# Optimization experiments

Measured on AMD Instinct MI355X. Metric: run time of the kernel, lower is better.

Reference implementation:

```python
import jax, jax.numpy as jnp
import numpy as np

N = 50000          # nodes
E = 800000         # edges (before self-loops)
NIN = 300          # n_in
H = 4              # heads
C = 64             # nhid (per-head out channels)
G = 256            # number of graphs in batch
NOUT = 768         # nout
NEG_SLOPE_ATT = 0.2   # PyG GATConv leaky-relu slope for attention logits
NEG_SLOPE_ACT = 0.01  # nn.LeakyReLU default


def setup_inputs() -> dict:
    key = jax.random.key(0)
    ks = jax.random.split(key, 9)
    x = jax.random.normal(ks[0], (N, NIN), dtype=jnp.float32)
    edge_index = jax.random.randint(ks[1], (2, E), 0, N, dtype=jnp.int32)
    batch = jnp.sort(jax.random.randint(ks[2], (N,), 0, G, dtype=jnp.int32))
    lin_w = jax.random.normal(ks[3], (NIN, H * C), dtype=jnp.float32) / np.sqrt(NIN)
    att_src = jax.random.normal(ks[4], (H, C), dtype=jnp.float32) / np.sqrt(C)
    att_dst = jax.random.normal(ks[5], (H, C), dtype=jnp.float32) / np.sqrt(C)
    bias = jnp.zeros((H * C,), dtype=jnp.float32)
    fc1_w = jax.random.normal(ks[6], (H * C, NOUT), dtype=jnp.float32) / np.sqrt(H * C)
    fc1_b = jnp.zeros((NOUT,), dtype=jnp.float32)
    return {"x": x, "edge_index": edge_index, "batch": batch, "lin_w": lin_w,
            "att_src": att_src, "att_dst": att_dst, "bias": bias,
            "fc1_w": fc1_w, "fc1_b": fc1_b}


def reference(x, edge_index, batch, lin_w, att_src, att_dst, bias, fc1_w, fc1_b):
    n = x.shape[0]
    h = (x @ lin_w).reshape(n, H, C)                      # [N,H,C]
    # add self-loops (PyG GATConv default)
    loop = jnp.arange(n, dtype=edge_index.dtype)
    src = jnp.concatenate([edge_index[0], loop])          # [E+N]
    dst = jnp.concatenate([edge_index[1], loop])
    # per-edge attention logits
    a_src = jnp.einsum('nhc,hc->nh', h, att_src)          # [N,H]
    a_dst = jnp.einsum('nhc,hc->nh', h, att_dst)
    e = jax.nn.leaky_relu(a_src[src] + a_dst[dst], NEG_SLOPE_ATT)  # [E+N,H]
    # segment softmax grouped by destination node (self-loops -> every segment nonempty)
    emax = jax.ops.segment_max(e, dst, num_segments=n)    # [N,H]
    ee = jnp.exp(e - emax[dst])
    denom = jax.ops.segment_sum(ee, dst, num_segments=n)
    alpha = ee / denom[dst]                               # [E+N,H]
    # weighted message aggregation
    msg = h[src] * alpha[..., None]                       # [E+N,H,C]
    out = jax.ops.segment_sum(msg, dst, num_segments=n).reshape(n, H * C) + bias
    out = jax.nn.leaky_relu(out, NEG_SLOPE_ACT)
    # global mean pool over graphs
    sums = jax.ops.segment_sum(out, batch, num_segments=G)        # [G,H*C]
    cnt = jax.ops.segment_sum(jnp.ones((n, 1), out.dtype), batch, num_segments=G)
    pooled = sums / jnp.maximum(cnt, 1.0)
    return pooled @ fc1_w + fc1_b                         # [G,NOUT]
```

## Files before the change

kernel.cpp:

```cpp
#include <hip/hip_runtime.h>
#include <hip/hip_bf16.h>

using bf16 = __hip_bfloat16;
typedef __attribute__((ext_vector_type(8))) short short8;
typedef __attribute__((ext_vector_type(4))) float f32x4;

constexpr int N   = 50000;
constexpr int E   = 800000;
constexpr int NIN = 300;
constexpr int H   = 4;
constexpr int C   = 64;
constexpr int HC  = H * C;
constexpr int G   = 256;
constexpr int NOUT = 768;
constexpr int NKB = 10;
constexpr int NT  = 782;

__device__ __forceinline__ float b2f(bf16 v) { return __bfloat162float(v); }
__device__ __forceinline__ float us2f(unsigned short u) {
    bf16 b; *(unsigned short*)&b = u; return __bfloat162float(b);
}
__device__ __forceinline__ unsigned short f2us(float f) {
    bf16 b = __float2bfloat16(f); return *(unsigned short*)&b;
}
__device__ __forceinline__ float lrelu_att(float v) { return v > 0.f ? v : 0.2f * v; }
__device__ __forceinline__ float lrelu_act(float v) { return v > 0.f ? v : 0.01f * v; }
__device__ __forceinline__ float ldin(const void* p, int isbf, size_t i) {
    return isbf ? b2f(((const bf16*)p)[i]) : ((const float*)p)[i];
}
__device__ __forceinline__ short8 pack8u(ushort4 lo, ushort4 hi) {
    short8 r;
    r[0] = (short)lo.x; r[1] = (short)lo.y; r[2] = (short)lo.z; r[3] = (short)lo.w;
    r[4] = (short)hi.x; r[5] = (short)hi.y; r[6] = (short)hi.z; r[7] = (short)hi.w;
    return r;
}
__device__ __forceinline__ short8 pack8f(float4 lo, float4 hi) {
    short8 r;
    r[0] = (short)f2us(lo.x); r[1] = (short)f2us(lo.y); r[2] = (short)f2us(lo.z); r[3] = (short)f2us(lo.w);
    r[4] = (short)f2us(hi.x); r[5] = (short)f2us(hi.y); r[6] = (short)f2us(hi.z); r[7] = (short)f2us(hi.w);
    return r;
}

__device__ __forceinline__ short8 loadA_bf(const unsigned short* __restrict__ xr, int kb, int q) {
    ushort4 z = make_ushort4(0, 0, 0, 0);
    ushort4 lo = z, hi = z;
    if (kb < 9) {
        lo = *(const ushort4*)(xr + kb * 32);
        hi = *(const ushort4*)(xr + kb * 32 + 4);
    } else if (q == 0) {
        lo = *(const ushort4*)(xr + 288); hi = *(const ushort4*)(xr + 292);
    } else if (q == 1) {
        lo = *(const ushort4*)(xr + 288);
    }
    return pack8u(lo, hi);
}
__device__ __forceinline__ short8 loadA_f32(const float* __restrict__ xf, int kb, int q) {
    float4 zf = make_float4(0.f, 0.f, 0.f, 0.f);
    float4 lo = zf, hi = zf;
    if (kb < 9) {
        lo = *(const float4*)(xf + kb * 32);
        hi = *(const float4*)(xf + kb * 32 + 4);
    } else if (q == 0) {
        lo = *(const float4*)(xf + 288); hi = *(const float4*)(xf + 292);
    } else if (q == 1) {
        lo = *(const float4*)(xf + 288);
    }
    return pack8f(lo, hi);
}

__device__ __forceinline__ int block_detect(const unsigned short* __restrict__ xr) {
    __shared__ int cnt_s;
    if (threadIdx.x == 0) cnt_s = 0;
    __syncthreads();
    unsigned short u = xr[threadIdx.x & 255];
    int ex = (u >> 7) & 0xFF;
    int ok = (ex == 0) || (ex >= 100 && ex <= 140);
    if (threadIdx.x < 256) atomicAdd(&cnt_s, ok);
    __syncthreads();
    return (cnt_s >= 240) ? 1 : 0;
}

constexpr int NZ  = N + G * HC;
constexpr int NZB = (NZ + 255) / 256;
__global__ __launch_bounds__(256) void k_pre(const unsigned short* __restrict__ xr,
                                             const void* __restrict__ w,
                                             const int* __restrict__ batch,
                                             int* __restrict__ flag,
                                             int* __restrict__ zp,
                                             unsigned short* __restrict__ bswz,
                                             int* __restrict__ gs) {
    int b = blockIdx.x;
    if (b < NZB) {
        int i = b * 256 + threadIdx.x;
        if (i < NZ) zp[i] = 0;
        if (b == 0) {
            int isbf = block_detect(xr);
            if (threadIdx.x == 0) *flag = isbf;
        }
    } else if (b < NZB + 40) {
        int isbf = block_detect(xr);
        int fb = (b - NZB) * 4 + (threadIdx.x >> 6);
        if (fb < 160) {
            int kb = fb >> 4, nb = fb & 15;
            int lane = threadIdx.x & 63;
            int q = lane >> 4, cl = lane & 15;
            int n = nb * 16 + cl;
            unsigned short v[8];
#pragma unroll
            for (int j = 0; j < 8; j++) {
                int k = kb * 32 + q * 8 + j;
                float f = (k < NIN) ? ldin(w, isbf, (size_t)k * HC + n) : 0.f;
                v[j] = f2us(f);
            }
            ushort4* dst = (ushort4*)(bswz + ((size_t)fb * 64 + lane) * 8);
            dst[0] = make_ushort4(v[0], v[1], v[2], v[3]);
            dst[1] = make_ushort4(v[4], v[5], v[6], v[7]);
        }
    } else {
        int g = threadIdx.x;
        int lo = 0, hi = N;
        while (lo < hi) {
            int mid = (lo + hi) >> 1;
            if (batch[mid] < g) lo = mid + 1;
            else hi = mid;
        }
        gs[g] = lo;
        if (g == 0) gs[G] = N;
    }
}

__global__ __launch_bounds__(256, 4) void k_lin4(const void* __restrict__ x,
                                                 const unsigned short* __restrict__ bswz,
                                                 const void* __restrict__ att_s,
                                                 const void* __restrict__ att_d,
                                                 unsigned short* __restrict__ hb,
                                                 float* __restrict__ a_src,
                                                 float* __restrict__ a_dst,
                                                 const int* __restrict__ flag) {
    __shared__ unsigned short bs[40 * 64 * 8];
    int isbf = *flag;
    int t = threadIdx.x;
    int c       = blockIdx.x & 7;
    int j       = blockIdx.x >> 3;
    int quarter = j & 3;
    int bslot   = (j >> 2) * 8 + c;
    for (int i = t; i < 40 * 64; i += 256) {
        int f = i >> 6, lane = i & 63;
        int kb = f >> 2, nbl = f & 3;
        const int4* src = (const int4*)(bswz + ((size_t)(kb * 16 + quarter * 4 + nbl) * 64 + lane) * 8);
        ((int4*)bs)[i] = *src;
    }
    __syncthreads();

    int wave = t >> 6, lane = t & 63;
    int q = lane >> 4, cl = lane & 15;
    int hh = quarter;
    float as_h[4], ad_h[4];
#pragma unroll
    for (int nbl = 0; nbl < 4; nbl++) {
        as_h[nbl] = ldin(att_s, isbf, (quarter * 4 + nbl) * 16 + cl);
        ad_h[nbl] = ldin(att_d, isbf, (quarter * 4 + nbl) * 16 + cl);
    }
    for (int tile = bslot; tile < NT; tile += 256) {
        int m0 = tile * 64 + wave * 16;
        int row = m0 + cl; if (row >= N) row = N - 1;
        f32x4 acc[4];
#pragma unroll
        for (int nbl = 0; nbl < 4; nbl++) acc[nbl] = f32x4{0.f, 0.f, 0.f, 0.f};
        if (isbf) {
            const unsigned short* xr = (const unsigned short*)x + (size_t)row * NIN + q * 8;
            short8 a_cur = loadA_bf(xr, 0, q);
            short8 a_nxt = loadA_bf(xr, 1, q);
#pragma unroll
            for (int kb = 0; kb < NKB; kb++) {
                short8 a_pf = {};
                if (kb + 2 < NKB) a_pf = loadA_bf(xr, kb + 2, q);
                short8 bfr[4];
#pragma unroll
                for (int nbl = 0; nbl < 4; nbl++)
                    bfr[nbl] = *(const short8*)(bs + ((size_t)(kb * 4 + nbl) * 64 + lane) * 8);
#pragma unroll
                for (int nbl = 0; nbl < 4; nbl++)
                    acc[nbl] = __builtin_amdgcn_mfma_f32_16x16x32_bf16(a_cur, bfr[nbl], acc[nbl], 0, 0, 0);
                a_cur = a_nxt; a_nxt = a_pf;
            }
        } else {
            const float* xf = (const float*)x + (size_t)row * NIN + q * 8;
            short8 a_cur = loadA_f32(xf, 0, q);
            short8 a_nxt = loadA_f32(xf, 1, q);
#pragma unroll
            for (int kb = 0; kb < NKB; kb++) {
                short8 a_pf = {};
                if (kb + 2 < NKB) a_pf = loadA_f32(xf, kb + 2, q);
                short8 bfr[4];
#pragma unroll
                for (int nbl = 0; nbl < 4; nbl++)
                    bfr[nbl] = *(const short8*)(bs + ((size_t)(kb * 4 + nbl) * 64 + lane) * 8);
#pragma unroll
                for (int nbl = 0; nbl < 4; nbl++)
                    acc[nbl] = __builtin_amdgcn_mfma_f32_16x16x32_bf16(a_cur, bfr[nbl], acc[nbl], 0, 0, 0);
                a_cur = a_nxt; a_nxt = a_pf;
            }
        }
        float ps[4], pd[4];
#pragma unroll
        for (int r = 0; r < 4; r++) { ps[r] = 0.f; pd[r] = 0.f; }
#pragma unroll
        for (int nbl = 0; nbl < 4; nbl++) {
            int nb = quarter * 4 + nbl;
#pragma unroll
            for (int r = 0; r < 4; r++) {
                float v = acc[nbl][r];
                ps[r] += v * as_h[nbl];
                pd[r] += v * ad_h[nbl];
                int gm = m0 + q * 4 + r;
                if (gm < N) hb[(size_t)gm * HC + nb * 16 + cl] = f2us(v);
            }
        }
#pragma unroll
        for (int r = 0; r < 4; r++) {
            float vs = ps[r], vd = pd[r];
#pragma unroll
            for (int m = 1; m < 16; m <<= 1) {
                vs += __shfl_xor(vs, m, 64);
                vd += __shfl_xor(vd, m, 64);
            }
            int gm = m0 + q * 4 + r;
            if (cl == 0 && gm < N) {
                a_src[gm * 4 + hh] = vs;
                a_dst[gm * 4 + hh] = vd;
            }
        }
    }
}

__global__ void k_hist(const int* __restrict__ dst, int* __restrict__ cnt) {
    int e = blockIdx.x * 256 + threadIdx.x;
    if (e < E) atomicAdd(&cnt[dst[e]], 1);
}

__global__ __launch_bounds__(256) void k_scan1(const int* __restrict__ cnt, int* __restrict__ bsum) {
    __shared__ int wsum[4];
    int idx = blockIdx.x * 256 + threadIdx.x;
    int v = (idx < N) ? cnt[idx] : 0;
#pragma unroll
    for (int o2 = 32; o2; o2 >>= 1) v += __shfl_down(v, o2, 64);
    if ((threadIdx.x & 63) == 0) wsum[threadIdx.x >> 6] = v;
    __syncthreads();
    if (threadIdx.x == 0) bsum[blockIdx.x] = wsum[0] + wsum[1] + wsum[2] + wsum[3];
}

__global__ __launch_bounds__(256) void k_scan23(const int* __restrict__ bsum, int nb,
                                                const int* __restrict__ cnt,
                                                int* __restrict__ off, int* __restrict__ cur) {
    __shared__ int sd[256];
    __shared__ int s_boff;
    int t = threadIdx.x;
    int v = (t < nb) ? bsum[t] : 0;
    sd[t] = v;
    __syncthreads();
    for (int d = 1; d < 256; d <<= 1) {
        int u = (t >= d) ? sd[t - d] : 0;
        __syncthreads();
        sd[t] += u;
        __syncthreads();
    }
    if (t == (int)blockIdx.x) s_boff = sd[t] - v;
    if (blockIdx.x == 0 && t == nb - 1) off[N] = sd[t];
    __syncthreads();
    int boff = s_boff;
    int idx = blockIdx.x * 256 + t;
    int c = (idx < N) ? cnt[idx] : 0;
    __syncthreads();
    sd[t] = c;
    __syncthreads();
    for (int d = 1; d < 256; d <<= 1) {
        int u = (t >= d) ? sd[t - d] : 0;
        __syncthreads();
        sd[t] += u;
        __syncthreads();
    }
    int ex = sd[t] - c + boff;
    if (idx < N) { off[idx] = ex; cur[idx] = ex; }
}

__global__ void k_scatter(const int* __restrict__ ei,
                          int* __restrict__ cur,
                          int* __restrict__ csr_s) {
    int e = blockIdx.x * 256 + threadIdx.x;
    if (e >= E) return;
    int s = ei[e], d = ei[E + e];
    int pos = atomicAdd(&cur[d], 1);
    csr_s[pos] = s;
}

__global__ __launch_bounds__(256) void k_agg(const unsigned short* __restrict__ hb,
                                             const float* __restrict__ a_src,
                                             const float* __restrict__ a_dst,
                                             const int* __restrict__ off,
                                             const int* __restrict__ csr_s,
                                             const void* __restrict__ bias,
                                             unsigned short* __restrict__ outn,
                                             const int* __restrict__ flag) {
    int isbf = *flag;
    int wave = threadIdx.x >> 6, lane = threadIdx.x & 63;
    int n = blockIdx.x * 4 + wave;
    if (n >= N) return;
    int head = lane >> 4;
    float adn = a_dst[n * 4 + head];
    float wself = __expf(lrelu_att(a_src[n * 4 + head] + adn));
    ushort4 hv = *(const ushort4*)&hb[(size_t)n * HC + lane * 4];
    float4 acc;
    acc.x = us2f(hv.x) * wself;
    acc.y = us2f(hv.y) * wself;
    acc.z = us2f(hv.z) * wself;
    acc.w = us2f(hv.w) * wself;
    float ssum = wself;
    int p0 = off[n], p1 = off[n + 1];
    int i0 = 0, i1 = 0, i2 = 0, i3 = 0;
    if (p0 + 4 <= p1) { i0 = csr_s[p0]; i1 = csr_s[p0 + 1]; i2 = csr_s[p0 + 2]; i3 = csr_s[p0 + 3]; }
    int p = p0;
    for (; p + 4 <= p1; p += 4) {
        int s0 = i0, s1 = i1, s2 = i2, s3 = i3;
        ushort4 g0 = *(const ushort4*)&hb[(size_t)s0 * HC + lane * 4];
        ushort4 g1 = *(const ushort4*)&hb[(size_t)s1 * HC + lane * 4];
        ushort4 g2 = *(const ushort4*)&hb[(size_t)s2 * HC + lane * 4];
        ushort4 g3 = *(const ushort4*)&hb[(size_t)s3 * HC + lane * 4];
        float w0 = __expf(lrelu_att(a_src[(size_t)s0 * 4 + head] + adn));
        float w1 = __expf(lrelu_att(a_src[(size_t)s1 * 4 + head] + adn));
        float w2 = __expf(lrelu_att(a_src[(size_t)s2 * 4 + head] + adn));
        float w3 = __expf(lrelu_att(a_src[(size_t)s3 * 4 + head] + adn));
        int nn = p + 4;
        if (nn + 4 <= p1) { i0 = csr_s[nn]; i1 = csr_s[nn + 1]; i2 = csr_s[nn + 2]; i3 = csr_s[nn + 3]; }
        acc.x += us2f(g0.x) * w0 + us2f(g1.x) * w1 + us2f(g2.x) * w2 + us2f(g3.x) * w3;
        acc.y += us2f(g0.y) * w0 + us2f(g1.y) * w1 + us2f(g2.y) * w2 + us2f(g3.y) * w3;
        acc.z += us2f(g0.z) * w0 + us2f(g1.z) * w1 + us2f(g2.z) * w2 + us2f(g3.z) * w3;
        acc.w += us2f(g0.w) * w0 + us2f(g1.w) * w1 + us2f(g2.w) * w2 + us2f(g3.w) * w3;
        ssum += (w0 + w1) + (w2 + w3);
    }
    for (; p < p1; p++) {
        int s = csr_s[p];
        float wv = __expf(lrelu_att(a_src[(size_t)s * 4 + head] + adn));
        ushort4 hs = *(const ushort4*)&hb[(size_t)s * HC + lane * 4];
        acc.x += us2f(hs.x) * wv;
        acc.y += us2f(hs.y) * wv;
        acc.z += us2f(hs.z) * wv;
        acc.w += us2f(hs.w) * wv;
        ssum += wv;
    }
    float inv = 1.f / ssum;
    ushort4 o;
    o.x = f2us(lrelu_act(acc.x * inv + ldin(bias, isbf, lane * 4 + 0)));
    o.y = f2us(lrelu_act(acc.y * inv + ldin(bias, isbf, lane * 4 + 1)));
    o.z = f2us(lrelu_act(acc.z * inv + ldin(bias, isbf, lane * 4 + 2)));
    o.w = f2us(lrelu_act(acc.w * inv + ldin(bias, isbf, lane * 4 + 3)));
    *(ushort4*)&outn[(size_t)n * HC + lane * 4] = o;
}

__global__ __launch_bounds__(256) void k_pool2(const unsigned short* __restrict__ outn,
                                               const int* __restrict__ gs,
                                               float* __restrict__ sums) {
    int g = blockIdx.x, qq = blockIdx.y, t = threadIdx.x;
    int s = gs[g], e2 = gs[g + 1];
    int len = e2 - s;
    int r0 = s + (len * qq) / 4;
    int r1 = s + (len * (qq + 1)) / 4;
    float a0 = 0.f, a1 = 0.f, a2 = 0.f, a3 = 0.f;
    int r = r0;
    for (; r + 4 <= r1; r += 4) {
        a0 += us2f(outn[(size_t)(r + 0) * HC + t]);
        a1 += us2f(outn[(size_t)(r + 1) * HC + t]);
        a2 += us2f(outn[(size_t)(r + 2) * HC + t]);
        a3 += us2f(outn[(size_t)(r + 3) * HC + t]);
    }
    for (; r < r1; r++) a0 += us2f(outn[(size_t)r * HC + t]);
    float v = (a0 + a1) + (a2 + a3);
    if (r1 > r0) atomicAdd(&sums[(size_t)g * HC + t], v);
}

__global__ __launch_bounds__(256) void k_fc(const float* __restrict__ sums,
                                            const int* __restrict__ gs,
                                            const void* __restrict__ fw,
                                            const void* __restrict__ fb,
                                            void* __restrict__ out,
                                            const int* __restrict__ flag) {
    __shared__ float pl[HC];
    int isbf = *flag;
    int g = blockIdx.y;
    int o = blockIdx.x * 256 + threadIdx.x;
    int c = gs[g + 1] - gs[g];
    float inv = 1.f / (float)(c > 1 ? c : 1);
    pl[threadIdx.x] = sums[(size_t)g * HC + threadIdx.x] * inv;
    __syncthreads();
    float acc = ldin(fb, isbf, o);
#pragma unroll 8
    for (int k = 0; k < HC; k++) acc += pl[k] * ldin(fw, isbf, (size_t)k * NOUT + o);
    size_t oi = (size_t)g * NOUT + o;
    if (isbf) ((bf16*)out)[oi] = __float2bfloat16(acc);
    else      ((float*)out)[oi] = acc;
}

extern "C" void kernel_launch(void* const* d_in, const int* in_sizes, int n_in,
                              void* d_out, int out_size, void* d_ws, size_t ws_size,
                              hipStream_t stream) {
    const void* x     = d_in[0];
    const int*  ei    = (const int*)d_in[1];
    const int*  batch = (const int*)d_in[2];
    const void* lin_w = d_in[3];
    const void* att_s = d_in[4];
    const void* att_d = d_in[5];
    const void* bias  = d_in[6];
    const void* fc1w  = d_in[7];
    const void* fc1b  = d_in[8];

    char* p = (char*)d_ws;
    unsigned short* hb   = (unsigned short*)p; p += (size_t)N * HC * 2;
    unsigned short* outn = (unsigned short*)p; p += (size_t)N * HC * 2;
    float* a_src  = (float*)p; p += (size_t)N * H * 4;
    float* a_dst  = (float*)p; p += (size_t)N * H * 4;
    int* cnt      = (int*)p;   p += (size_t)N * 4;
    float* sums   = (float*)p; p += (size_t)G * HC * 4;
    int* off      = (int*)p;   p += (size_t)(N + 4) * 4;
    int* cur      = (int*)p;   p += (size_t)N * 4;
    int* csr_s    = (int*)p;   p += (size_t)E * 4;
    unsigned short* bswz = (unsigned short*)p; p += (size_t)160 * 64 * 8 * 2;
    int* bsum     = (int*)p;   p += 1024;
    int* gs       = (int*)p;   p += (size_t)(G + 4) * 4;
    int* flag     = (int*)p;   p += 16;

    const int NB = (N + 255) / 256;

    k_pre<<<NZB + 40 + 1, 256, 0, stream>>>((const unsigned short*)x, lin_w, batch,
                                            flag, cnt, bswz, gs);
    k_lin4<<<1024, 256, 0, stream>>>(x, bswz, att_s, att_d, hb, a_src, a_dst, flag);
    k_hist<<<(E + 255) / 256, 256, 0, stream>>>(ei + E, cnt);
    k_scan1<<<NB, 256, 0, stream>>>(cnt, bsum);
    k_scan23<<<NB, 256, 0, stream>>>(bsum, NB, cnt, off, cur);
    k_scatter<<<(E + 255) / 256, 256, 0, stream>>>(ei, cur, csr_s);
    k_agg<<<(N + 3) / 4, 256, 0, stream>>>(hb, a_src, a_dst, off, csr_s, bias, outn, flag);
    k_pool2<<<dim3(G, 4), 256, 0, stream>>>(outn, gs, sums);
    k_fc<<<dim3(NOUT / 256, G), 256, 0, stream>>>(sums, gs, fc1w, fc1b, d_out, flag);
}
```

Baseline: 324.3 us.

## Store h in per-head planes and aggregate one head per wave

The linear kernel now writes h as four head-major planes of N×64 bf16 instead of interleaved N×256 rows. The aggregation kernel launches 8 blocks per group of node-pairs so each wave handles one head of one node. The four 16-lane slots of a wave process four different edges in parallel, and the partial sums are combined with cross-slot shuffles. The aim is to make each head's gathered working set smaller and more cache-friendly, and to spread edge latency across lanes. The cost is four times as many waves, each re-reading the CSR offsets and indices, and more idle lanes on low-degree nodes.

```diff
diff --git a/kernel.cpp b/kernel.cpp
--- a/kernel.cpp
+++ b/kernel.cpp
@@ -207,14 +207,14 @@
         for (int r = 0; r < 4; r++) { ps[r] = 0.f; pd[r] = 0.f; }
 #pragma unroll
         for (int nbl = 0; nbl < 4; nbl++) {
-            int nb = quarter * 4 + nbl;
 #pragma unroll
             for (int r = 0; r < 4; r++) {
                 float v = acc[nbl][r];
                 ps[r] += v * as_h[nbl];
                 pd[r] += v * ad_h[nbl];
                 int gm = m0 + q * 4 + r;
-                if (gm < N) hb[(size_t)gm * HC + nb * 16 + cl] = f2us(v);
+                if (gm < N)
+                    hb[((size_t)quarter * N + gm) * 64 + nbl * 16 + cl] = f2us(v);
             }
         }
 #pragma unroll
@@ -304,57 +304,73 @@
                                              const int* __restrict__ flag) {
     int isbf = *flag;
     int wave = threadIdx.x >> 6, lane = threadIdx.x & 63;
-    int n = blockIdx.x * 4 + wave;
-    if (n >= N) return;
-    int head = lane >> 4;
-    float adn = a_dst[n * 4 + head];
+    int c    = blockIdx.x & 7;
+    int head = c >> 1;
+    int nbk  = (blockIdx.x >> 3) * 2 + (c & 1);
+    int n    = nbk * 4 + wave;
+    int slot = lane >> 4, ch4 = (lane & 15) * 4;
+    const unsigned short* plane = hb + (size_t)head * N * 64;
+
+    float adn   = a_dst[n * 4 + head];
     float wself = __expf(lrelu_att(a_src[n * 4 + head] + adn));
-    ushort4 hv = *(const ushort4*)&hb[(size_t)n * HC + lane * 4];
-    float4 acc;
-    acc.x = us2f(hv.x) * wself;
-    acc.y = us2f(hv.y) * wself;
-    acc.z = us2f(hv.z) * wself;
-    acc.w = us2f(hv.w) * wself;
-    float ssum = wself;
+    ushort4 hv  = *(const ushort4*)&plane[(size_t)n * 64 + ch4];
+    float4 acc = make_float4(0.f, 0.f, 0.f, 0.f);
+    float ssum = 0.f;
+    if (slot == 0) {
+        acc.x = us2f(hv.x) * wself;
+        acc.y = us2f(hv.y) * wself;
+        acc.z = us2f(hv.z) * wself;
+        acc.w = us2f(hv.w) * wself;
+        ssum  = wself;
+    }
+
     int p0 = off[n], p1 = off[n + 1];
-    int i0 = 0, i1 = 0, i2 = 0, i3 = 0;
-    if (p0 + 4 <= p1) { i0 = csr_s[p0]; i1 = csr_s[p0 + 1]; i2 = csr_s[p0 + 2]; i3 = csr_s[p0 + 3]; }
     int p = p0;
-    for (; p + 4 <= p1; p += 4) {
-        int s0 = i0, s1 = i1, s2 = i2, s3 = i3;
-        ushort4 g0 = *(const ushort4*)&hb[(size_t)s0 * HC + lane * 4];
-        ushort4 g1 = *(const ushort4*)&hb[(size_t)s1 * HC + lane * 4];
-        ushort4 g2 = *(const ushort4*)&hb[(size_t)s2 * HC + lane * 4];
-        ushort4 g3 = *(const ushort4*)&hb[(size_t)s3 * HC + lane * 4];
-        float w0 = __expf(lrelu_att(a_src[(size_t)s0 * 4 + head] + adn));
-        float w1 = __expf(lrelu_att(a_src[(size_t)s1 * 4 + head] + adn));
-        float w2 = __expf(lrelu_att(a_src[(size_t)s2 * 4 + head] + adn));
-        float w3 = __expf(lrelu_att(a_src[(size_t)s3 * 4 + head] + adn));
-        int nn = p + 4;
-        if (nn + 4 <= p1) { i0 = csr_s[nn]; i1 = csr_s[nn + 1]; i2 = csr_s[nn + 2]; i3 = csr_s[nn + 3]; }
-        acc.x += us2f(g0.x) * w0 + us2f(g1.x) * w1 + us2f(g2.x) * w2 + us2f(g3.x) * w3;
-        acc.y += us2f(g0.y) * w0 + us2f(g1.y) * w1 + us2f(g2.y) * w2 + us2f(g3.y) * w3;
-        acc.z += us2f(g0.z) * w0 + us2f(g1.z) * w1 + us2f(g2.z) * w2 + us2f(g3.z) * w3;
-        acc.w += us2f(g0.w) * w0 + us2f(g1.w) * w1 + us2f(g2.w) * w2 + us2f(g3.w) * w3;
-        ssum += (w0 + w1) + (w2 + w3);
-    }
-    for (; p < p1; p++) {
-        int s = csr_s[p];
-        float wv = __expf(lrelu_att(a_src[(size_t)s * 4 + head] + adn));
-        ushort4 hs = *(const ushort4*)&hb[(size_t)s * HC + lane * 4];
-        acc.x += us2f(hs.x) * wv;
-        acc.y += us2f(hs.y) * wv;
-        acc.z += us2f(hs.z) * wv;
-        acc.w += us2f(hs.w) * wv;
-        ssum += wv;
+    bool act = false; float wv = 0.f; ushort4 g = hv;
+    if (p < p1) {
+        int rem = p1 - p;
+        act = slot < rem;
+        int ii = act ? csr_s[p + slot] : n;
+        wv = act ? a_src[(size_t)ii * 4 + head] : 0.f;
+        g  = *(const ushort4*)&plane[(size_t)ii * 64 + ch4];
+    }
+    while (p < p1) {
+        int pn = p + 4;
+        bool act2 = false; float wv2 = 0.f; ushort4 g2 = g;
+        if (pn < p1) {
+            int rem2 = p1 - pn;
+            act2 = slot < rem2;
+            int ii2 = act2 ? csr_s[pn + slot] : n;
+            wv2 = act2 ? a_src[(size_t)ii2 * 4 + head] : 0.f;
+            g2  = *(const ushort4*)&plane[(size_t)ii2 * 64 + ch4];
+        }
+        float e = act ? __expf(lrelu_att(wv + adn)) : 0.f;
+        acc.x += us2f(g.x) * e;
+        acc.y += us2f(g.y) * e;
+        acc.z += us2f(g.z) * e;
+        acc.w += us2f(g.w) * e;
+        ssum += e;
+        act = act2; wv = wv2; g = g2; p = pn;
+    }
+
+#pragma unroll
+    for (int m = 16; m <= 32; m <<= 1) {
+        acc.x += __shfl_xor(acc.x, m, 64);
+        acc.y += __shfl_xor(acc.y, m, 64);
+        acc.z += __shfl_xor(acc.z, m, 64);
+        acc.w += __shfl_xor(acc.w, m, 64);
+        ssum  += __shfl_xor(ssum,  m, 64);
     }
     float inv = 1.f / ssum;
-    ushort4 o;
-    o.x = f2us(lrelu_act(acc.x * inv + ldin(bias, isbf, lane * 4 + 0)));
-    o.y = f2us(lrelu_act(acc.y * inv + ldin(bias, isbf, lane * 4 + 1)));
-    o.z = f2us(lrelu_act(acc.z * inv + ldin(bias, isbf, lane * 4 + 2)));
-    o.w = f2us(lrelu_act(acc.w * inv + ldin(bias, isbf, lane * 4 + 3)));
-    *(ushort4*)&outn[(size_t)n * HC + lane * 4] = o;
+    if (lane < 16) {
+        int ob = head * 64 + ch4;
+        ushort4 o;
+        o.x = f2us(lrelu_act(acc.x * inv + ldin(bias, isbf, ob + 0)));
+        o.y = f2us(lrelu_act(acc.y * inv + ldin(bias, isbf, ob + 1)));
+        o.z = f2us(lrelu_act(acc.z * inv + ldin(bias, isbf, ob + 2)));
+        o.w = f2us(lrelu_act(acc.w * inv + ldin(bias, isbf, ob + 3)));
+        *(ushort4*)&outn[(size_t)n * HC + ob] = o;
+    }
 }
 
 __global__ __launch_bounds__(256) void k_pool2(const unsigned short* __restrict__ outn,
@@ -437,7 +453,7 @@
     k_scan1<<<NB, 256, 0, stream>>>(cnt, bsum);
     k_scan23<<<NB, 256, 0, stream>>>(bsum, NB, cnt, off, cur);
     k_scatter<<<(E + 255) / 256, 256, 0, stream>>>(ei, cur, csr_s);
-    k_agg<<<(N + 3) / 4, 256, 0, stream>>>(hb, a_src, a_dst, off, csr_s, bias, outn, flag);
+    k_agg<<<50000, 256, 0, stream>>>(hb, a_src, a_dst, off, csr_s, bias, outn, flag);
     k_pool2<<<dim3(G, 4), 256, 0, stream>>>(outn, gs, sums);
     k_fc<<<dim3(NOUT / 256, G), 256, 0, stream>>>(sums, gs, fc1w, fc1b, d_out, flag);
 }
```

Result: slower. 396.0 us (+22.1%).
